# Optimization experiments

Measured on AMD Instinct MI355X. Metric: run time of the kernel, lower is better.

Reference implementation:

```python
import jax, jax.numpy as jnp
import numpy as np

N = 20000      # atom nodes
N_LG = 40000   # line-graph nodes (= undirected bonds)
E = 80000      # directed edges in original graph (= 2*N_LG)
E_LG = 200000  # line-graph edges
L = 5          # num_layer
D = 300        # emb_dim
NUM_ATOM, NUM_BOND, NUM_DIR, NUM_CHI = 120, 6, 3, 3
EPS = 1e-5


def setup_inputs() -> dict:
    key = jax.random.key(0)
    ks = jax.random.split(key, 24)
    ri = lambda k, shape, hi: jax.random.randint(k, shape, 0, hi, dtype=jnp.int32)
    nm = lambda k, shape: jax.random.normal(k, shape, dtype=jnp.float32) * 0.02
    inp = {}
    inp["x"] = ri(ks[0], (N, 2), 3)
    inp["edge_index"] = ri(ks[1], (2, E), N)
    inp["edge_attr"] = ri(ks[2], (E, 2), 3)
    inp["lg_x"] = ri(ks[3], (N_LG, 2), 3)
    inp["lg_edge_index"] = ri(ks[4], (2, E_LG), N_LG)
    inp["lg_edge_index_map"] = ri(ks[5], (2, N_LG), N)
    inp["lg_edge_index_map2"] = ri(ks[6], (E_LG,), N)
    # GNN-level embeddings
    inp["node_emb1"] = nm(ks[7], (NUM_ATOM, D))
    inp["node_emb2"] = nm(ks[8], (NUM_CHI, D))
    inp["gnn_edge_emb1"] = nm(ks[9], (NUM_BOND, D))
    inp["gnn_edge_emb2"] = nm(ks[10], (NUM_DIR, D))
    # per-layer main-graph GINConv params (stacked over layers)
    inp["g_emb1"] = nm(ks[11], (L, NUM_BOND, D))
    inp["g_emb2"] = nm(ks[12], (L, NUM_DIR, D))
    inp["g_w1"] = nm(ks[13], (L, D, 2 * D))
    inp["g_b1"] = jnp.zeros((L, 2 * D), jnp.float32)
    inp["g_w2"] = nm(ks[14], (L, 2 * D, D))
    inp["g_b2"] = jnp.zeros((L, D), jnp.float32)
    inp["g_gamma"] = jnp.ones((L, D), jnp.float32)
    inp["g_beta"] = jnp.zeros((L, D), jnp.float32)
    # per-layer line-graph GINConv params (is_lg=True -> atom/chirality tables)
    inp["lg_emb1"] = nm(ks[15], (L, NUM_ATOM, D))
    inp["lg_emb2"] = nm(ks[16], (L, NUM_CHI, D))
    inp["lg_w1"] = nm(ks[17], (L, D, 2 * D))
    inp["lg_b1"] = jnp.zeros((L, 2 * D), jnp.float32)
    inp["lg_w2"] = nm(ks[18], (L, 2 * D, D))
    inp["lg_b2"] = jnp.zeros((L, D), jnp.float32)
    inp["lg_gamma"] = jnp.ones((L, D), jnp.float32)
    inp["lg_beta"] = jnp.zeros((L, D), jnp.float32)
    return inp


def gin_conv(xn, src, dst, ea, emb1, emb2, sl_idx, w1, b1, w2, b2):
    # self loops appended at the end, with self_loop_attr = emb1[sl_idx] + emb2[0]
    n = xn.shape[0]
    sl = jnp.broadcast_to(emb1[sl_idx] + emb2[0], (n, xn.shape[1]))
    ea_full = jnp.concatenate([ea, sl], axis=0)
    idx = jnp.arange(n, dtype=src.dtype)
    src_f = jnp.concatenate([src, idx])
    dst_f = jnp.concatenate([dst, idx])
    msg = xn[src_f] + ea_full                      # gather + add
    aggr = jax.ops.segment_sum(msg, dst_f, num_segments=n)  # scatter-add
    return jnp.maximum(aggr @ w1 + b1, 0.0) @ w2 + b2        # MLP update


def batchnorm(h, g, b):
    # training-mode BN: batch mean / biased variance (matches torch normalization)
    mu = h.mean(0)
    var = h.var(0)
    return (h - mu) * jax.lax.rsqrt(var + EPS) * g + b


def reference(x, edge_index, edge_attr, lg_x, lg_edge_index, lg_edge_index_map,
              lg_edge_index_map2, node_emb1, node_emb2, gnn_edge_emb1, gnn_edge_emb2,
              g_emb1, g_emb2, g_w1, g_b1, g_w2, g_b2, g_gamma, g_beta,
              lg_emb1, lg_emb2, lg_w1, lg_b1, lg_w2, lg_b2, lg_gamma, lg_beta):
    h = node_emb1[x[:, 0]] + node_emb2[x[:, 1]]
    e = gnn_edge_emb1[lg_x[:, 0]] + gnn_edge_emb2[lg_x[:, 1]]
    h_list, e_list = [h], [e]
    lg_src, lg_dst = lg_edge_index[0], lg_edge_index[1]
    for layer in range(L):
        if layer == 0:
            ea = g_emb1[0][edge_attr[:, 0]] + g_emb2[0][edge_attr[:, 1]]
            src, dst = edge_index[0], edge_index[1]
        else:
            # edge_index rewritten from line-graph map; edge_attr = cat([e, e])
            ea = jnp.concatenate([e_list[layer], e_list[layer]], axis=0)
            src = jnp.concatenate([lg_edge_index_map[0], lg_edge_index_map[1]])
            dst = jnp.concatenate([lg_edge_index_map[1], lg_edge_index_map[0]])
        h = gin_conv(h_list[layer], src, dst, ea, g_emb1[layer], g_emb2[layer], 4,
                     g_w1[layer], g_b1[layer], g_w2[layer], g_b2[layer])
        h = batchnorm(h, g_gamma[layer], g_beta[layer])
        if layer < L - 1:
            h = jnp.maximum(h, 0.0)
        h_list.append(h)
        if layer == 0:
            xa = x[lg_edge_index_map2]  # int atom features of shared node
            lg_ea = lg_emb1[0][xa[:, 0]] + lg_emb2[0][xa[:, 1]]
        else:
            # lg_edge_attr = h[lg_edge_index_map2] from the PREVIOUS iteration's h
            lg_ea = h_list[layer][lg_edge_index_map2]
        e = gin_conv(e_list[layer], lg_src, lg_dst, lg_ea, lg_emb1[layer], lg_emb2[layer], 119,
                     lg_w1[layer], lg_b1[layer], lg_w2[layer], lg_b2[layer])
        e = batchnorm(e, lg_gamma[layer], lg_beta[layer])
        if layer < L - 1:
            e = jnp.maximum(e, 0.0)
        e_list.append(e)
    # (h_list, e_list) packed as one array: [L+1, N + N_LG, D]
    return jnp.concatenate([jnp.stack(h_list), jnp.stack(e_list)], axis=1)
```

## Files before the change

kernel.cpp:

```cpp
#include <hip/hip_runtime.h>

#define D 300

namespace {

constexpr int kN   = 20000;
constexpr int kNLG = 40000;
constexpr int kE   = 80000;
constexpr int kELG = 200000;
constexpr int kL   = 5;

constexpr int K1P = 320;
constexpr int N1P = 640;
constexpr int K2P = 640;
constexpr int N2P = 384;
constexpr int PQH = 320;
constexpr int MP_N   = 20096;
constexpr int MP_ALL = 60160;
constexpr int MAIN_TILES = 157;
constexpr int RH = 320;
constexpr int RQ = 40;
constexpr int NALL = kN + kNLG;

typedef __attribute__((ext_vector_type(8))) _Float16 half8;
typedef __attribute__((ext_vector_type(2))) _Float16 half2v;
typedef __attribute__((ext_vector_type(4))) float f32x4;

__device__ inline short f2h(float f) {
  _Float16 h = (_Float16)f;
  return __builtin_bit_cast(short, h);
}

__device__ inline float2 upk(unsigned u) {
  half2v h = __builtin_bit_cast(half2v, u);
  return make_float2((float)h.x, (float)h.y);
}

__device__ inline unsigned pk(float a, float b) {
  half2v h;
  h.x = (_Float16)a;
  h.y = (_Float16)b;
  return __builtin_bit_cast(unsigned, h);
}

__device__ inline void addrow(float* acc, uint4 r) {
  float2 t0 = upk(r.x), t1 = upk(r.y), t2 = upk(r.z), t3 = upk(r.w);
  acc[0] += t0.x; acc[1] += t0.y; acc[2] += t1.x; acc[3] += t1.y;
  acc[4] += t2.x; acc[5] += t2.y; acc[6] += t3.x; acc[7] += t3.y;
}

__device__ inline void unpk8(uint4 r, float* v) {
  float2 t0 = upk(r.x), t1 = upk(r.y), t2 = upk(r.z), t3 = upk(r.w);
  v[0] = t0.x; v[1] = t0.y; v[2] = t1.x; v[3] = t1.y;
  v[4] = t2.x; v[5] = t2.y; v[6] = t3.x; v[7] = t3.y;
}

__device__ inline uint4 pk4(const float* a) {
  uint4 r;
  r.x = pk(a[0], a[1]); r.y = pk(a[2], a[3]);
  r.z = pk(a[4], a[5]); r.w = pk(a[6], a[7]);
  return r;
}

__device__ inline void gload_lds16(const void* g, void* l) {
  __builtin_amdgcn_global_load_lds(
      (const __attribute__((address_space(1))) void*)g,
      (__attribute__((address_space(3))) void*)l, 16, 0, 0);
}


__global__ void k_init(float* __restrict__ stats, short* __restrict__ ab,
                       int* __restrict__ m0_cur, int* __restrict__ mL_cur,
                       int* __restrict__ lg_cur) {
  int g = blockIdx.x * blockDim.x + threadIdx.x;
  if (g < kL * 1200) stats[g] = 0.f;
  int np1 = (MP_N - kN) * K1P;
  int np2 = (MP_ALL - MP_N - kNLG) * K1P;
  if (g < np1) ab[(size_t)kN * K1P + g] = 0;
  if (g < np2) ab[(size_t)(MP_N + kNLG) * K1P + g] = 0;
  if (g < kN) { m0_cur[g] = 0; mL_cur[g] = 0; }
  if (g < kNLG) lg_cur[g] = 0;
}


__global__ void k_hist_all(const int* __restrict__ edge_index,
                           const int* __restrict__ lg_map,
                           const int* __restrict__ lg_ei,
                           const int* __restrict__ eattr,
                           const int* __restrict__ map2,
                           const int* __restrict__ x,
                           int* __restrict__ m0_cur, int* __restrict__ mL_cur,
                           int* __restrict__ lg_cur,
                           int* __restrict__ cam, int* __restrict__ cal) {
  int g = blockIdx.x * blockDim.x + threadIdx.x;
  if (g < kE) {
    atomicAdd(&m0_cur[edge_index[kE + g]], 1);
    cam[g] = eattr[2 * g] * 3 + eattr[2 * g + 1];
    return;
  }
  g -= kE;
  if (g < kNLG) { atomicAdd(&mL_cur[lg_map[kNLG + g]], 1); return; }
  g -= kNLG;
  if (g < kNLG) { atomicAdd(&mL_cur[lg_map[g]], 1); return; }
  g -= kNLG;
  if (g < kELG) {
    atomicAdd(&lg_cur[lg_ei[kELG + g]], 1);
    int a = map2[g];
    cal[g] = x[2 * a] * 3 + x[2 * a + 1];
  }
}

__device__ void scan_one(int* cursor, int* offs, int n) {
  __shared__ int part[256];
  int tid = threadIdx.x;
  int chunk = (n + 255) / 256;
  int s0 = tid * chunk;
  int s1 = min(n, s0 + chunk);
  int sum = 0;
  for (int i = s0; i < s1; ++i) sum += cursor[i];
  part[tid] = sum;
  __syncthreads();
  for (int off = 1; off < 256; off <<= 1) {
    int v = (tid >= off) ? part[tid - off] : 0;
    __syncthreads();
    part[tid] += v;
    __syncthreads();
  }
  int run = (tid == 0) ? 0 : part[tid - 1];
  for (int i = s0; i < s1; ++i) {
    int dv = cursor[i];
    offs[i] = run;
    cursor[i] = run;
    run += dv;
  }
  if (tid == 255) offs[n] = run;
}

__global__ __launch_bounds__(256) void k_scan3(
    int* __restrict__ m0_cur, int* __restrict__ m0_offs,
    int* __restrict__ mL_cur, int* __restrict__ mL_offs,
    int* __restrict__ lg_cur, int* __restrict__ lg_offs) {
  if (blockIdx.x == 0) scan_one(m0_cur, m0_offs, kN);
  else if (blockIdx.x == 1) scan_one(mL_cur, mL_offs, kN);
  else scan_one(lg_cur, lg_offs, kNLG);
}

__global__ void k_fill_all(const int* __restrict__ edge_index,
                           const int* __restrict__ lg_map,
                           const int* __restrict__ lg_ei,
                           int* __restrict__ m0_cur, int* __restrict__ m0_perm,
                           int* __restrict__ mL_cur, int* __restrict__ mL_perm,
                           int* __restrict__ lg_cur, int* __restrict__ lg_perm) {
  int g = blockIdx.x * blockDim.x + threadIdx.x;
  if (g < kE) {
    int pos = atomicAdd(&m0_cur[edge_index[kE + g]], 1);
    m0_perm[pos] = g;
    return;
  }
  g -= kE;
  if (g < kNLG) {
    int pos = atomicAdd(&mL_cur[lg_map[kNLG + g]], 1);
    mL_perm[pos] = g;
    return;
  }
  g -= kNLG;
  if (g < kNLG) {
    int pos = atomicAdd(&mL_cur[lg_map[g]], 1);
    mL_perm[pos] = kNLG + g;
    return;
  }
  g -= kNLG;
  if (g < kELG) {
    int pos = atomicAdd(&lg_cur[lg_ei[kELG + g]], 1);
    lg_perm[pos] = g;
  }
}


__global__ void k_selfvec(const float* __restrict__ g1, const float* __restrict__ g2,
                          const float* __restrict__ l1, const float* __restrict__ l2,
                          float* __restrict__ slv) {
  int g = blockIdx.x * blockDim.x + threadIdx.x;
  if (g >= kL * 640) return;
  int l = g / 640, rem = g - l * 640;
  int gr = rem / 320, c = rem - gr * 320;
  float v = 0.f;
  if (c < D) {
    if (gr == 0) v = g1[(size_t)l * 6 * D + 4 * D + c] + g2[(size_t)l * 3 * D + c];
    else         v = l1[(size_t)l * 120 * D + 119 * D + c] + l2[(size_t)l * 3 * D + c];
  }
  slv[g] = v;
}

__global__ void k_comb_tab(const float* __restrict__ g1, const float* __restrict__ g2,
                           const float* __restrict__ l1, const float* __restrict__ l2,
                           short* __restrict__ tcm, short* __restrict__ tcl) {
  int g = blockIdx.x * blockDim.x + threadIdx.x;
  if (g < 18 * RH) {
    int p = g / RH, c = g - p * RH;
    float v = (c < D) ? g1[(size_t)(p / 3) * D + c] + g2[(size_t)(p % 3) * D + c] : 0.f;
    tcm[g] = f2h(v);
    return;
  }
  g -= 18 * RH;
  if (g < 360 * RH) {
    int p = g / RH, c = g - p * RH;
    float v = (c < D) ? l1[(size_t)(p / 3) * D + c] + l2[(size_t)(p % 3) * D + c] : 0.f;
    tcl[g] = f2h(v);
  }
}

__device__ void cvt_w1(const float* W, short* Wt, int g) {
  int per = N1P * K1P;
  int l = g / per, rem = g - l * per;
  int n = rem / K1P, k = rem - n * K1P;
  float v = (n < 2 * D && k < D) ? W[(size_t)l * D * 2 * D + (size_t)k * 2 * D + n] : 0.f;
  Wt[g] = f2h(v);
}

__device__ void cvt_w2(const float* W, short* Wt, int g) {
  int per = N2P * K2P;
  int l = g / per, rem = g - l * per;
  int n = rem / K2P, k = rem - n * K2P;
  float v = (n < D && k < 2 * D) ? W[(size_t)l * 2 * D * D + (size_t)k * D + n] : 0.f;
  Wt[g] = f2h(v);
}

__global__ void k_convert_wt_all(const float* __restrict__ g_w1, const float* __restrict__ g_w2,
                                 const float* __restrict__ lg_w1, const float* __restrict__ lg_w2,
                                 short* __restrict__ g_w1t, short* __restrict__ g_w2t,
                                 short* __restrict__ lg_w1t, short* __restrict__ lg_w2t) {
  int g = blockIdx.x * blockDim.x + threadIdx.x;
  const int s1 = kL * N1P * K1P, s2 = kL * N2P * K2P;
  if (g < s1) { cvt_w1(g_w1, g_w1t, g); return; }
  g -= s1;
  if (g < s2) { cvt_w2(g_w2, g_w2t, g); return; }
  g -= s2;
  if (g < s1) { cvt_w1(lg_w1, lg_w1t, g); return; }
  g -= s1;
  if (g < s2) cvt_w2(lg_w2, lg_w2t, g);
}


__global__ void k_embed_all(const int* __restrict__ x, const int* __restrict__ lg_x,
                            const float* __restrict__ t1m, const float* __restrict__ t2m,
                            const float* __restrict__ t1l, const float* __restrict__ t2l,
                            float* __restrict__ outF, uint4* __restrict__ hist) {
  int g = blockIdx.x * blockDim.x + threadIdx.x;
  if (g >= NALL * RQ) return;
  int r = g / RQ, q = g - r * RQ;
  bool m = r < kN;
  int i = m ? r : r - kN;
  const int* ix = (m ? x : lg_x) + 2 * i;
  const float* t1 = (m ? t1m : t1l) + (size_t)ix[0] * D;
  const float* t2 = (m ? t2m : t2l) + (size_t)ix[1] * D;
  int c0 = q * 8;
  float y[8] = {0.f, 0.f, 0.f, 0.f, 0.f, 0.f, 0.f, 0.f};
  if (c0 < D) {
    float4 p0 = *(const float4*)(t1 + c0);
    float4 q0 = *(const float4*)(t2 + c0);
    y[0] = p0.x + q0.x; y[1] = p0.y + q0.y; y[2] = p0.z + q0.z; y[3] = p0.w + q0.w;
    *(float4*)(outF + (size_t)r * D + c0) = make_float4(y[0], y[1], y[2], y[3]);
    if (c0 + 8 <= D) {
      float4 p1 = *(const float4*)(t1 + c0 + 4);
      float4 q1 = *(const float4*)(t2 + c0 + 4);
      y[4] = p1.x + q1.x; y[5] = p1.y + q1.y; y[6] = p1.z + q1.z; y[7] = p1.w + q1.w;
      *(float4*)(outF + (size_t)r * D + c0 + 4) = make_float4(y[4], y[5], y[6], y[7]);
    }
  }
  hist[(size_t)r * RQ + q] = pk4(y);
}


#define GATHER_BODY                                                     \
  int p0 = offs[j], p1 = offs[j + 1];                                   \
  for (int pb = p0; pb < p1; pb += 64) {                                \
    int cnt = min(64, p1 - pb);                                         \
    int e_ = permp[pb + ((lane < cnt) ? lane : 0)];                     \
    int ra, rb;                                                         \
    GATHER_IDX                                                          \
    for (int t = 0; t < cnt; t += 8) {                                  \
      uint4 xa[8], xb[8];                                               \
      _Pragma("unroll")                                                 \
      for (int u = 0; u < 8; ++u) {                                     \
        int tt = min(t + u, cnt - 1);                                   \
        int a0 = __shfl(ra, tt), b0 = __shfl(rb, tt);                   \
        xa[u] = bA[(size_t)a0 * RQ + ll];                               \
        xb[u] = bB[(size_t)b0 * RQ + ll];                               \
      }                                                                 \
      int lim = min(8, cnt - t);                                        \
      _Pragma("unroll")                                                 \
      for (int u = 0; u < 8; ++u)                                       \
        if (u < lim) { addrow(acc, xa[u]); addrow(acc, xb[u]); }        \
    }                                                                   \
  }

__global__ void k_gather_all0(
    const uint4* __restrict__ h16, const uint4* __restrict__ e16,
    const int* __restrict__ m_src, const int* __restrict__ lg_src,
    const int* __restrict__ cam, const int* __restrict__ cal,
    const uint4* __restrict__ tcm, const uint4* __restrict__ tcl,
    const float* __restrict__ slvM, const float* __restrict__ slvL,
    const int* __restrict__ m_offs, const int* __restrict__ m_perm,
    const int* __restrict__ l_offs, const int* __restrict__ l_perm,
    uint4* __restrict__ ab) {
  int node = blockIdx.x * 4 + (threadIdx.x >> 6);
  int lane = threadIdx.x & 63;
  if (node >= NALL) return;
  bool act = lane < RQ;
  int ll = act ? lane : 0;
  bool isM = node < kN;
  int j = isM ? node : node - kN;
  const uint4* selfrow = isM ? (h16 + (size_t)node * RQ) : (e16 + (size_t)j * RQ);
  const float* sv = (isM ? slvM : slvL) + ll * 8;
  const int* offs = isM ? m_offs : l_offs;
  const int* permp = isM ? m_perm : l_perm;
  const uint4* bA = isM ? h16 : e16;
  const uint4* bB = isM ? tcm : tcl;
  const int* srcp = isM ? m_src : lg_src;
  const int* catp = isM ? cam : cal;

  float acc[8];
  {
    float vv[8];
    unpk8(selfrow[ll], vv);
#pragma unroll
    for (int i = 0; i < 8; ++i) acc[i] = vv[i] + sv[i];
  }

#define GATHER_IDX ra = srcp[e_]; rb = catp[e_];
  GATHER_BODY
#undef GATHER_IDX

  if (act) ab[(size_t)(isM ? node : MP_N + j) * RQ + ll] = pk4(acc);
}

__global__ void k_gather_allL(
    const uint4* __restrict__ h16, const uint4* __restrict__ e16,
    const int* __restrict__ lg_map, const int* __restrict__ lg_src,
    const int* __restrict__ map2,
    const float* __restrict__ slvM, const float* __restrict__ slvL,
    const int* __restrict__ m_offs, const int* __restrict__ m_perm,
    const int* __restrict__ l_offs, const int* __restrict__ l_perm,
    uint4* __restrict__ ab) {
  int node = blockIdx.x * 4 + (threadIdx.x >> 6);
  int lane = threadIdx.x & 63;
  if (node >= NALL) return;
  bool act = lane < RQ;
  int ll = act ? lane : 0;
  bool isM = node < kN;
  int j = isM ? node : node - kN;
  const uint4* selfrow = isM ? (h16 + (size_t)node * RQ) : (e16 + (size_t)j * RQ);
  const float* sv = (isM ? slvM : slvL) + ll * 8;
  const int* offs = isM ? m_offs : l_offs;
  const int* permp = isM ? m_perm : l_perm;
  const uint4* bA = isM ? h16 : e16;
  const uint4* bB = isM ? e16 : h16;

  float acc[8];
  {
    float vv[8];
    unpk8(selfrow[ll], vv);
#pragma unroll
    for (int i = 0; i < 8; ++i) acc[i] = vv[i] + sv[i];
  }

#define GATHER_IDX                                     \
  if (isM) {                                           \
    ra = lg_map[e_];                                   \
    rb = (e_ < kNLG) ? e_ : e_ - kNLG;                 \
  } else {                                             \
    ra = lg_src[e_];                                   \
    rb = map2[e_];                                     \
  }
  GATHER_BODY
#undef GATHER_IDX

  if (act) ab[(size_t)(isM ? node : MP_N + j) * RQ + ll] = pk4(acc);
}


template<bool RELU, bool STATS>
__global__ __launch_bounds__(256) void k_mfma_gemm_dual(
    const short* __restrict__ A,
    const short* __restrict__ BtM, const short* __restrict__ BtL,
    const float* __restrict__ biasM, const float* __restrict__ biasL, int biasN,
    short* __restrict__ Cout, int Cstat, int Cwrite, int Cstride, int Kpad,
    int mainLimit, int lgLimit,
    float* __restrict__ statsM, float* __restrict__ statsL) {
  __shared__ __align__(16) short ldsA[128 * 32];
  __shared__ __align__(16) short ldsB[128 * 32];
  __shared__ float sd[256];
  const int tid = threadIdx.x;
  const int lane = tid & 63, w = tid >> 6;
  const bool isMain = (int)blockIdx.y < MAIN_TILES;
  const short* Bt = isMain ? BtM : BtL;
  const float* bias = isMain ? biasM : biasL;
  const int rowLimit = isMain ? mainLimit : lgLimit;
  const int brow = blockIdx.y * 128;
  const int bcol = blockIdx.x * 128;
  const int wr = w >> 1, wc = w & 1;

  if (STATS) sd[tid] = 0.f;

  f32x4 acc[4][4] = {};

  const int sr = tid >> 2;
  const int sc = (tid & 3) * 8;
  char* la = (char*)ldsA + w * 1024;
  char* lb = (char*)ldsB + w * 1024;

  for (int k0 = 0; k0 < Kpad; k0 += 32) {
    __syncthreads();
    const short* gA0 = A + (size_t)(brow + sr) * Kpad + (k0 + sc);
    const short* gB0 = Bt + (size_t)(bcol + sr) * Kpad + (k0 + sc);
    gload_lds16(gA0, la);
    gload_lds16(gA0 + (size_t)64 * Kpad, la + 4096);
    gload_lds16(gB0, lb);
    gload_lds16(gB0 + (size_t)64 * Kpad, lb + 4096);
    __syncthreads();

    const int kq = (lane >> 4) * 16;
    half8 af[4], bf[4];
#pragma unroll
    for (int m = 0; m < 4; ++m) {
      int row = wr * 64 + m * 16 + (lane & 15);
      af[m] = *(const half8*)((const char*)ldsA + row * 64 + kq);
    }
#pragma unroll
    for (int n = 0; n < 4; ++n) {
      int col = wc * 64 + n * 16 + (lane & 15);
      bf[n] = *(const half8*)((const char*)ldsB + col * 64 + kq);
    }
#pragma unroll
    for (int m = 0; m < 4; ++m)
#pragma unroll
      for (int n = 0; n < 4; ++n)
        acc[m][n] = __builtin_amdgcn_mfma_f32_16x16x32_f16(af[m], bf[n], acc[m][n], 0, 0, 0);
  }

  const int r0 = brow + wr * 64;
  const int c0 = bcol + wc * 64;
  float ps[4] = {}, pq[4] = {};
#pragma unroll
  for (int m = 0; m < 4; ++m) {
#pragma unroll
    for (int i = 0; i < 4; ++i) {
      int row = r0 + m * 16 + (lane >> 4) * 4 + i;
      bool rv = row < rowLimit;
#pragma unroll
      for (int n = 0; n < 4; ++n) {
        int col = c0 + n * 16 + (lane & 15);
        float bv = (col < biasN) ? bias[col] : 0.f;
        float v = acc[m][n][i] + bv;
        if (RELU) v = fmaxf(v, 0.f);
        if (rv && col < Cwrite) {
          Cout[(size_t)row * Cstride + col] = f2h(v);
          if (STATS && col < Cstat) { ps[n] += v; pq[n] += v * v; }
        }
      }
    }
  }

  if (STATS) {
#pragma unroll
    for (int n = 0; n < 4; ++n) {
      float s = ps[n], q = pq[n];
      s += __shfl_xor(s, 16); q += __shfl_xor(q, 16);
      s += __shfl_xor(s, 32); q += __shfl_xor(q, 32);
      if ((lane >> 4) == 0) {
        int c = wc * 64 + n * 16 + (lane & 15);
        atomicAdd(&sd[c], s);
        atomicAdd(&sd[128 + c], q);
      }
    }
    __syncthreads();
    float* gs = isMain ? statsM : statsL;
    if (tid < 128) {
      int col = bcol + tid;
      if (col < Cstat) {
        atomicAdd(&gs[col], sd[tid]);
        atomicAdd(&gs[D + col], sd[128 + tid]);
      }
    }
  }
}


__global__ void k_bn_coef(const float* __restrict__ stats,
                          const float* __restrict__ gM, const float* __restrict__ bM,
                          const float* __restrict__ gL, const float* __restrict__ bL,
                          float* __restrict__ coef) {
  int t = blockIdx.x * blockDim.x + threadIdx.x;
  if (t >= 640) return;
  bool m = t < 320;
  int c = m ? t : t - 320;
  float a = 0.f, b = 0.f;
  if (c < D) {
    const float* s = stats + (m ? 0 : 600);
    float inv_n = m ? (1.f / kN) : (1.f / kNLG);
    float mu = s[c] * inv_n;
    float var = s[D + c] * inv_n - mu * mu;
    a = rsqrtf(var + 1e-5f) * (m ? gM : gL)[c];
    b = (m ? bM : bL)[c] - mu * a;
  }
  int base = m ? 0 : 640;
  coef[base + c] = a;
  coef[base + 320 + c] = b;
}


template<bool RELU, bool WRITE_HIST>
__global__ void k_bn_apply_v(const uint4* __restrict__ pre, const float* __restrict__ coef,
                             float* __restrict__ outF, uint4* __restrict__ hist) {
  int g = blockIdx.x * blockDim.x + threadIdx.x;
  if (g >= NALL * RQ) return;
  int r = g / RQ, q = g - r * RQ;
  bool m = r < kN;
  int pr = m ? r : MP_N + (r - kN);
  float v[8], y[8];
  unpk8(pre[(size_t)pr * RQ + q], v);
  const float* cb = coef + (m ? 0 : 640);
  float4 a0 = *(const float4*)(cb + q * 8);
  float4 a1 = *(const float4*)(cb + q * 8 + 4);
  float4 b0 = *(const float4*)(cb + 320 + q * 8);
  float4 b1 = *(const float4*)(cb + 320 + q * 8 + 4);
  y[0] = a0.x * v[0] + b0.x; y[1] = a0.y * v[1] + b0.y;
  y[2] = a0.z * v[2] + b0.z; y[3] = a0.w * v[3] + b0.w;
  y[4] = a1.x * v[4] + b1.x; y[5] = a1.y * v[5] + b1.y;
  y[6] = a1.z * v[6] + b1.z; y[7] = a1.w * v[7] + b1.w;
  if (RELU) {
#pragma unroll
    for (int i = 0; i < 8; ++i) y[i] = fmaxf(y[i], 0.f);
  }
  float* op = outF + (size_t)r * D + q * 8;
  if (q < 37) {
    *(float4*)op = make_float4(y[0], y[1], y[2], y[3]);
    *(float4*)(op + 4) = make_float4(y[4], y[5], y[6], y[7]);
  } else if (q == 37) {
    *(float4*)op = make_float4(y[0], y[1], y[2], y[3]);
  }
  if (WRITE_HIST) hist[(size_t)r * RQ + q] = pk4(y);
}

}

extern "C" void kernel_launch(void* const* d_in, const int* in_sizes, int n_in,
                              void* d_out_v, int out_size, void* d_ws, size_t ws_size,
                              hipStream_t stream) {
  const int*   x            = (const int*)d_in[0];
  const int*   edge_index   = (const int*)d_in[1];
  const int*   edge_attr    = (const int*)d_in[2];
  const int*   lg_x         = (const int*)d_in[3];
  const int*   lg_edge_index= (const int*)d_in[4];
  const int*   lg_map       = (const int*)d_in[5];
  const int*   lg_map2      = (const int*)d_in[6];
  const float* node_emb1    = (const float*)d_in[7];
  const float* node_emb2    = (const float*)d_in[8];
  const float* gnn_e_emb1   = (const float*)d_in[9];
  const float* gnn_e_emb2   = (const float*)d_in[10];
  const float* g_emb1       = (const float*)d_in[11];
  const float* g_emb2       = (const float*)d_in[12];
  const float* g_w1         = (const float*)d_in[13];
  const float* g_b1         = (const float*)d_in[14];
  const float* g_w2         = (const float*)d_in[15];
  const float* g_b2         = (const float*)d_in[16];
  const float* g_gamma      = (const float*)d_in[17];
  const float* g_beta       = (const float*)d_in[18];
  const float* lg_emb1      = (const float*)d_in[19];
  const float* lg_emb2      = (const float*)d_in[20];
  const float* lg_w1        = (const float*)d_in[21];
  const float* lg_b1        = (const float*)d_in[22];
  const float* lg_w2        = (const float*)d_in[23];
  const float* lg_b2        = (const float*)d_in[24];
  const float* lg_gamma     = (const float*)d_in[25];
  const float* lg_beta      = (const float*)d_in[26];

  float* out = (float*)d_out_v;
  char*  ws  = (char*)d_ws;

  size_t off = 0;
  auto alloc = [&](size_t bytes) { void* p = ws + off; off = (off + bytes + 255) & ~(size_t)255; return p; };
  short* ab      = (short*)alloc((size_t)MP_ALL * K1P * 2);
  short* hidden  = (short*)alloc((size_t)MP_ALL * N1P * 2);
  short* pre16   = (short*)alloc((size_t)MP_ALL * PQH * 2);
  short* hist2   = (short*)alloc((size_t)2 * NALL * RH * 2);
  short* g_w1t   = (short*)alloc((size_t)kL * N1P * K1P * 2);
  short* g_w2t   = (short*)alloc((size_t)kL * N2P * K2P * 2);
  short* lg_w1t  = (short*)alloc((size_t)kL * N1P * K1P * 2);
  short* lg_w2t  = (short*)alloc((size_t)kL * N2P * K2P * 2);
  float* stats   = (float*)alloc(kL * 1200 * 4);
  float* slv     = (float*)alloc(kL * 640 * 4);
  float* coef    = (float*)alloc(1280 * 4);
  short* tcm     = (short*)alloc(18 * RH * 2);
  short* tcl     = (short*)alloc(360 * RH * 2);
  int* cam     = (int*)alloc(kE * 4);
  int* cal     = (int*)alloc(kELG * 4);
  int* m0_offs = (int*)alloc((kN + 1) * 4);
  int* m0_cur  = (int*)alloc(kN * 4);
  int* m0_perm = (int*)alloc(kE * 4);
  int* mL_offs = (int*)alloc((kN + 1) * 4);
  int* mL_cur  = (int*)alloc(kN * 4);
  int* mL_perm = (int*)alloc(2 * kNLG * 4);
  int* lg_offs = (int*)alloc((kNLG + 1) * 4);
  int* lg_cur  = (int*)alloc(kNLG * 4);
  int* lg_perm = (int*)alloc(kELG * 4);

  auto hptr = [&](int l) { return out + (size_t)l * 60000 * D; };
  auto slot_h = [&](int s) { return hist2 + (size_t)s * NALL * RH; };
  auto slot_e = [&](int s) { return hist2 + (size_t)s * NALL * RH + (size_t)kN * RH; };

  dim3 b(256);

  k_init<<<(kNLG + 255) / 256, b, 0, stream>>>(stats, ab, m0_cur, mL_cur, lg_cur);
  {
    int tot = kE + 2 * kNLG + kELG;
    k_hist_all<<<(tot + 255) / 256, b, 0, stream>>>(edge_index, lg_map, lg_edge_index,
                                                    edge_attr, lg_map2, x,
                                                    m0_cur, mL_cur, lg_cur, cam, cal);
    k_scan3<<<3, b, 0, stream>>>(m0_cur, m0_offs, mL_cur, mL_offs, lg_cur, lg_offs);
    k_fill_all<<<(tot + 255) / 256, b, 0, stream>>>(edge_index, lg_map, lg_edge_index,
                                                    m0_cur, m0_perm, mL_cur, mL_perm,
                                                    lg_cur, lg_perm);
  }
  k_selfvec<<<(kL * 640 + 255) / 256, b, 0, stream>>>(g_emb1, g_emb2, lg_emb1, lg_emb2, slv);
  k_comb_tab<<<(378 * RH + 255) / 256, b, 0, stream>>>(g_emb1, g_emb2, lg_emb1, lg_emb2,
                                                       tcm, tcl);
  {
    int tot = 2 * kL * (N1P * K1P + N2P * K2P);
    k_convert_wt_all<<<(tot + 255) / 256, b, 0, stream>>>(g_w1, g_w2, lg_w1, lg_w2,
                                                          g_w1t, g_w2t, lg_w1t, lg_w2t);
  }
  k_embed_all<<<(NALL * RQ + 255) / 256, b, 0, stream>>>(x, lg_x, node_emb1, node_emb2,
                                                         gnn_e_emb1, gnn_e_emb2,
                                                         hptr(0), (uint4*)slot_h(0));

  int cur = 0;
  for (int l = 0; l < kL; ++l) {
    float* slot = stats + (size_t)l * 1200;
    const float* slvM = slv + (size_t)l * 640;
    const float* slvL = slvM + 320;

    if (l == 0)
      k_gather_all0<<<(NALL + 3) / 4, b, 0, stream>>>(
          (const uint4*)slot_h(cur), (const uint4*)slot_e(cur),
          edge_index, lg_edge_index, cam, cal,
          (const uint4*)tcm, (const uint4*)tcl,
          slvM, slvL, m0_offs, m0_perm, lg_offs, lg_perm, (uint4*)ab);
    else
      k_gather_allL<<<(NALL + 3) / 4, b, 0, stream>>>(
          (const uint4*)slot_h(cur), (const uint4*)slot_e(cur),
          lg_map, lg_edge_index, lg_map2,
          slvM, slvL, mL_offs, mL_perm, lg_offs, lg_perm, (uint4*)ab);

    k_mfma_gemm_dual<true, false><<<dim3(N1P / 128, MP_ALL / 128), b, 0, stream>>>(
        ab, g_w1t + (size_t)l * N1P * K1P, lg_w1t + (size_t)l * N1P * K1P,
        g_b1 + (size_t)l * 2 * D, lg_b1 + (size_t)l * 2 * D, 2 * D,
        hidden, 0, N1P, N1P, K1P, MP_ALL, MP_ALL, nullptr, nullptr);

    k_mfma_gemm_dual<false, true><<<dim3(N2P / 128, MP_ALL / 128), b, 0, stream>>>(
        hidden, g_w2t + (size_t)l * N2P * K2P, lg_w2t + (size_t)l * N2P * K2P,
        g_b2 + (size_t)l * D, lg_b2 + (size_t)l * D, D,
        pre16, D, PQH, PQH, K2P, kN, MP_N + kNLG,
        slot, slot + 600);

    k_bn_coef<<<3, b, 0, stream>>>(slot,
                                   g_gamma + (size_t)l * D, g_beta + (size_t)l * D,
                                   lg_gamma + (size_t)l * D, lg_beta + (size_t)l * D, coef);

    int nxt = cur ^ 1;
    if (l < kL - 1)
      k_bn_apply_v<true, true><<<(NALL * RQ + 255) / 256, b, 0, stream>>>(
          (const uint4*)pre16, coef, hptr(l + 1), (uint4*)slot_h(nxt));
    else
      k_bn_apply_v<false, false><<<(NALL * RQ + 255) / 256, b, 0, stream>>>(
          (const uint4*)pre16, coef, hptr(l + 1), (uint4*)slot_h(nxt));
    cur = nxt;
  }
}
```

Before: 1.483 ms.

## Double-buffer GEMM LDS tiles, remap blocks per XCD, trim padded K and gather unroll

The MFMA GEMM now double-buffers its LDS A/B tiles so the global-to-LDS load of the next K slice overlaps the MFMAs on the current one, with one barrier per iteration. It also uses a 1D grid whose block index is remapped so consecutive row tiles land on the same XCD and share the weight columns in cache. Padding work is trimmed: the first GEMM writes only 608 of 640 hidden columns and the second loops K only to 608, skipping zero-padded K slices. The gather loop drops from an 8-wide clamped unroll to a 4-wide unroll plus a scalar tail. The cost is doubled LDS per block and less memory-level parallelism in the gather.

```diff
diff --git a/kernel.cpp b/kernel.cpp
--- a/kernel.cpp
+++ b/kernel.cpp
@@ -18,6 +18,8 @@
 constexpr int MP_N   = 20096;
 constexpr int MP_ALL = 60160;
 constexpr int MAIN_TILES = 157;
+constexpr int NRT = 470;
+constexpr int NRP = 59;
 constexpr int RH = 320;
 constexpr int RQ = 40;
 constexpr int NALL = kN + kNLG;
@@ -279,19 +281,30 @@
     int e_ = permp[pb + ((lane < cnt) ? lane : 0)];                     \
     int ra, rb;                                                         \
     GATHER_IDX                                                          \
-    for (int t = 0; t < cnt; t += 8) {                                  \
-      uint4 xa[8], xb[8];                                               \
-      _Pragma("unroll")                                                 \
-      for (int u = 0; u < 8; ++u) {                                     \
-        int tt = min(t + u, cnt - 1);                                   \
-        int a0 = __shfl(ra, tt), b0 = __shfl(rb, tt);                   \
-        xa[u] = bA[(size_t)a0 * RQ + ll];                               \
-        xb[u] = bB[(size_t)b0 * RQ + ll];                               \
-      }                                                                 \
-      int lim = min(8, cnt - t);                                        \
-      _Pragma("unroll")                                                 \
-      for (int u = 0; u < 8; ++u)                                       \
-        if (u < lim) { addrow(acc, xa[u]); addrow(acc, xb[u]); }        \
+    int t = 0;                                                          \
+    for (; t + 3 < cnt; t += 4) {                                       \
+      int a0 = __shfl(ra, t),     b0 = __shfl(rb, t);                   \
+      int a1 = __shfl(ra, t + 1), b1 = __shfl(rb, t + 1);               \
+      int a2 = __shfl(ra, t + 2), b2 = __shfl(rb, t + 2);               \
+      int a3 = __shfl(ra, t + 3), b3 = __shfl(rb, t + 3);               \
+      uint4 x0 = bA[(size_t)a0 * RQ + ll];                              \
+      uint4 y0 = bB[(size_t)b0 * RQ + ll];                              \
+      uint4 x1 = bA[(size_t)a1 * RQ + ll];                              \
+      uint4 y1 = bB[(size_t)b1 * RQ + ll];                              \
+      uint4 x2 = bA[(size_t)a2 * RQ + ll];                              \
+      uint4 y2 = bB[(size_t)b2 * RQ + ll];                              \
+      uint4 x3 = bA[(size_t)a3 * RQ + ll];                              \
+      uint4 y3 = bB[(size_t)b3 * RQ + ll];                              \
+      addrow(acc, x0); addrow(acc, y0);                                 \
+      addrow(acc, x1); addrow(acc, y1);                                 \
+      addrow(acc, x2); addrow(acc, y2);                                 \
+      addrow(acc, x3); addrow(acc, y3);                                 \
+    }                                                                   \
+    for (; t < cnt; ++t) {                                              \
+      int a0 = __shfl(ra, t), b0 = __shfl(rb, t);                       \
+      uint4 x0 = bA[(size_t)a0 * RQ + ll];                              \
+      uint4 y0 = bB[(size_t)b0 * RQ + ll];                              \
+      addrow(acc, x0); addrow(acc, y0);                                 \
     }                                                                   \
   }
 
@@ -385,20 +398,30 @@
     const short* __restrict__ A,
     const short* __restrict__ BtM, const short* __restrict__ BtL,
     const float* __restrict__ biasM, const float* __restrict__ biasL, int biasN,
-    short* __restrict__ Cout, int Cstat, int Cwrite, int Cstride, int Kpad,
+    short* __restrict__ Cout, int Cstat, int Cwrite, int Cstride,
+    int Astride, int Kloop, int NC,
     int mainLimit, int lgLimit,
     float* __restrict__ statsM, float* __restrict__ statsL) {
-  __shared__ __align__(16) short ldsA[128 * 32];
-  __shared__ __align__(16) short ldsB[128 * 32];
+  __shared__ __align__(16) short ldsA[2][128 * 32];
+  __shared__ __align__(16) short ldsB[2][128 * 32];
   __shared__ float sd[256];
+
+  int bid = blockIdx.x;
+  int xcd = bid & 7;
+  int t0 = bid >> 3;
+  int c = t0 % NC;
+  int rr = t0 / NC;
+  int rtile = rr * 8 + xcd;
+  if (rtile >= NRT) return;
+
   const int tid = threadIdx.x;
   const int lane = tid & 63, w = tid >> 6;
-  const bool isMain = (int)blockIdx.y < MAIN_TILES;
+  const bool isMain = rtile < MAIN_TILES;
   const short* Bt = isMain ? BtM : BtL;
   const float* bias = isMain ? biasM : biasL;
   const int rowLimit = isMain ? mainLimit : lgLimit;
-  const int brow = blockIdx.y * 128;
-  const int bcol = blockIdx.x * 128;
+  const int brow = rtile * 128;
+  const int bcol = c * 128;
   const int wr = w >> 1, wc = w & 1;
 
   if (STATS) sd[tid] = 0.f;
@@ -407,36 +430,46 @@
 
   const int sr = tid >> 2;
   const int sc = (tid & 3) * 8;
-  char* la = (char*)ldsA + w * 1024;
-  char* lb = (char*)ldsB + w * 1024;
-
-  for (int k0 = 0; k0 < Kpad; k0 += 32) {
-    __syncthreads();
-    const short* gA0 = A + (size_t)(brow + sr) * Kpad + (k0 + sc);
-    const short* gB0 = Bt + (size_t)(bcol + sr) * Kpad + (k0 + sc);
+
+  auto stage = [&](int buf, int k0) {
+    char* la = (char*)(&ldsA[buf][0]) + w * 1024;
+    char* lb = (char*)(&ldsB[buf][0]) + w * 1024;
+    const short* gA0 = A + (size_t)(brow + sr) * Astride + (k0 + sc);
+    const short* gB0 = Bt + (size_t)(bcol + sr) * Astride + (k0 + sc);
     gload_lds16(gA0, la);
-    gload_lds16(gA0 + (size_t)64 * Kpad, la + 4096);
+    gload_lds16(gA0 + (size_t)64 * Astride, la + 4096);
     gload_lds16(gB0, lb);
-    gload_lds16(gB0 + (size_t)64 * Kpad, lb + 4096);
-    __syncthreads();
+    gload_lds16(gB0 + (size_t)64 * Astride, lb + 4096);
+  };
+
+  const int nt = Kloop / 32;
+  stage(0, 0);
+  __syncthreads();
+
+  for (int t = 0; t < nt; ++t) {
+    int cb = t & 1;
+    if (t + 1 < nt) stage(cb ^ 1, (t + 1) * 32);
 
     const int kq = (lane >> 4) * 16;
+    const char* baseA = (const char*)(&ldsA[cb][0]);
+    const char* baseB = (const char*)(&ldsB[cb][0]);
     half8 af[4], bf[4];
 #pragma unroll
     for (int m = 0; m < 4; ++m) {
       int row = wr * 64 + m * 16 + (lane & 15);
-      af[m] = *(const half8*)((const char*)ldsA + row * 64 + kq);
+      af[m] = *(const half8*)(baseA + row * 64 + kq);
     }
 #pragma unroll
     for (int n = 0; n < 4; ++n) {
       int col = wc * 64 + n * 16 + (lane & 15);
-      bf[n] = *(const half8*)((const char*)ldsB + col * 64 + kq);
+      bf[n] = *(const half8*)(baseB + col * 64 + kq);
     }
 #pragma unroll
     for (int m = 0; m < 4; ++m)
 #pragma unroll
       for (int n = 0; n < 4; ++n)
         acc[m][n] = __builtin_amdgcn_mfma_f32_16x16x32_f16(af[m], bf[n], acc[m][n], 0, 0, 0);
+    __syncthreads();
   }
 
   const int r0 = brow + wr * 64;
@@ -469,9 +502,9 @@
       s += __shfl_xor(s, 16); q += __shfl_xor(q, 16);
       s += __shfl_xor(s, 32); q += __shfl_xor(q, 32);
       if ((lane >> 4) == 0) {
-        int c = wc * 64 + n * 16 + (lane & 15);
-        atomicAdd(&sd[c], s);
-        atomicAdd(&sd[128 + c], q);
+        int cc = wc * 64 + n * 16 + (lane & 15);
+        atomicAdd(&sd[cc], s);
+        atomicAdd(&sd[128 + cc], q);
       }
     }
     __syncthreads();
@@ -653,15 +686,15 @@
           lg_map, lg_edge_index, lg_map2,
           slvM, slvL, mL_offs, mL_perm, lg_offs, lg_perm, (uint4*)ab);
 
-    k_mfma_gemm_dual<true, false><<<dim3(N1P / 128, MP_ALL / 128), b, 0, stream>>>(
+    k_mfma_gemm_dual<true, false><<<8 * NRP * 5, b, 0, stream>>>(
         ab, g_w1t + (size_t)l * N1P * K1P, lg_w1t + (size_t)l * N1P * K1P,
         g_b1 + (size_t)l * 2 * D, lg_b1 + (size_t)l * 2 * D, 2 * D,
-        hidden, 0, N1P, N1P, K1P, MP_ALL, MP_ALL, nullptr, nullptr);
-
-    k_mfma_gemm_dual<false, true><<<dim3(N2P / 128, MP_ALL / 128), b, 0, stream>>>(
+        hidden, 0, 608, N1P, K1P, K1P, 5, MP_ALL, MP_ALL, nullptr, nullptr);
+
+    k_mfma_gemm_dual<false, true><<<8 * NRP * 3, b, 0, stream>>>(
         hidden, g_w2t + (size_t)l * N2P * K2P, lg_w2t + (size_t)l * N2P * K2P,
         g_b2 + (size_t)l * D, lg_b2 + (size_t)l * D, D,
-        pre16, D, PQH, PQH, K2P, kN, MP_N + kNLG,
+        pre16, D, PQH, PQH, K2P, 608, 3, kN, MP_N + kNLG,
         slot, slot + 600);
 
     k_bn_coef<<<3, b, 0, stream>>>(slot,
```

Result: faster. 1.397 ms (-5.8%).
